# Kernel optimization log

Hardware: AMD Instinct MI355X
Metric: run time of the kernel (lower is better)

Reference implementation:

```python
import jax, jax.numpy as jnp
import numpy as np

B, T, F, U4 = 4096, 72, 64, 1024  # U4 = 4*units, units=256


def setup_inputs() -> dict:
    key = jax.random.key(0)
    ks = jax.random.split(key, 5)
    return {
        "inputs": jax.random.normal(ks[0], (B, T, F), jnp.float32),
        "W": jax.random.normal(ks[1], (F, U4), jnp.float32) * 0.05,   # input kernel [F, 4U]
        "U": jax.random.normal(ks[2], (U4 // 4, U4), jnp.float32) * 0.05,  # recurrent kernel [U, 4U]
        "b": jnp.zeros((U4,), jnp.float32),
        "Wd": jax.random.normal(ks[3], (U4 // 4, F), jnp.float32) * 0.05,  # dense [U, F]
        "bd": jnp.zeros((F,), jnp.float32),
        "out_steps": 24,
    }


def _lstm_step(h, c, x, W, U, b):
    # Keras LSTMCell gate order: i, f, g(candidate), o
    z = x @ W + h @ U + b  # [B, 4U]
    i, f, g, o = jnp.split(z, 4, axis=-1)
    i = jax.nn.sigmoid(i)
    f = jax.nn.sigmoid(f)
    o = jax.nn.sigmoid(o)
    c_new = f * c + i * jnp.tanh(g)
    h_new = o * jnp.tanh(c_new)
    return h_new, c_new


def reference(inputs, W, U, b, Wd, bd, out_steps):
    units = U.shape[0]
    Bt = inputs.shape[0]
    h0 = jnp.zeros((Bt, units), inputs.dtype)
    c0 = jnp.zeros((Bt, units), inputs.dtype)

    # ---- warmup: run RNN over the input sequence ----
    def warm_body(carry, x_t):
        h, c = carry
        h, c = _lstm_step(h, c, x_t, W, U, b)
        return (h, c), None

    (h, c), _ = jax.lax.scan(warm_body, (h0, c0), jnp.swapaxes(inputs, 0, 1))
    pred0 = h @ Wd + bd  # [B, F]

    def dec_body(carry, _):
        pred, h, c = carry
        h, c = _lstm_step(h, c, pred, W, U, b)
        pred = h @ Wd + bd
        return (pred, h, c), pred

    _, preds_rest = jax.lax.scan(dec_body, (pred0, h, c), None, length=out_steps - 1)
    preds = jnp.concatenate([pred0[None], preds_rest], axis=0)  # [out_steps, B, F]
    return jnp.transpose(preds, (1, 0, 2))  # [B, out_steps, F]
```

## Files before the change

kernel.cpp:

```cpp
#include <hip/hip_runtime.h>
#include <math.h>

constexpr int SEQ_T = 72;
constexpr int FDIM  = 64;
constexpr int UNITS = 256;
constexpr int U4    = 1024;
constexpr int BATCH = 4096;
constexpr int NKC   = 10;


constexpr int A_SH    = NKC * 4 * 64 * 8;
constexpr int WL_SH   = 6 * 4 * 4 * 64 * 8;
constexpr int HST_SH  = 2 * 4 * 64 * 8;
constexpr int LDS_BYTES = (A_SH + WL_SH + HST_SH) * 2;

using bf16x8 = __attribute__((ext_vector_type(8))) short;
using f32x4  = __attribute__((ext_vector_type(4))) float;

__device__ __forceinline__ float sigmoid_fast(float x) {
    return 1.0f / (1.0f + __expf(-x));
}
__device__ __forceinline__ float tanh_fast(float x) {
    float ax = fabsf(x);
    float e  = __expf(2.0f * ax);
    float t  = 1.0f - 2.0f / (e + 1.0f);
    return copysignf(t, x);
}
__device__ __forceinline__ unsigned short f2bf(float f) {
    union { float f; unsigned u; } v; v.f = f;
    unsigned r = (v.u + 0x7FFFu + ((v.u >> 16) & 1u)) >> 16;
    return (unsigned short)r;
}
__device__ __forceinline__ bf16x8 pack8(float4 a, float4 b) {
    bf16x8 p;
    p[0] = (short)f2bf(a.x); p[1] = (short)f2bf(a.y);
    p[2] = (short)f2bf(a.z); p[3] = (short)f2bf(a.w);
    p[4] = (short)f2bf(b.x); p[5] = (short)f2bf(b.y);
    p[6] = (short)f2bf(b.z); p[7] = (short)f2bf(b.w);
    return p;
}

__global__ void prep_wblob(const float* __restrict__ W, const float* __restrict__ U,
                           unsigned short* __restrict__ Wblob) {
    int id = blockIdx.x * 256 + threadIdx.x;
    int l    = id & 63;
    int g    = (id >> 6) & 3;
    int ug   = (id >> 8) & 3;
    int rest = id >> 10;
    int kc   = rest % 10, ub = rest / 10;
    int col  = g * 256 + ub * 64 + ug * 16 + (l & 15);
    int kb   = kc * 32 + (l >> 4) * 8;
    bf16x8 v;
    #pragma unroll
    for (int e = 0; e < 8; ++e) {
        int k = kb + e;
        float f = (k < FDIM) ? W[(size_t)k * U4 + col] : U[(size_t)(k - FDIM) * U4 + col];
        v[e] = (short)f2bf(f);
    }
    *reinterpret_cast<bf16x8*>(Wblob + (size_t)id * 8) = v;
}

__global__ void prep_wdblob(const float* __restrict__ Wd, unsigned short* __restrict__ Wdblob) {
    int id = blockIdx.x * 256 + threadIdx.x;
    int l   = id & 63;
    int kcd = (id >> 6) & 7;
    int ft  = id >> 9;
    int f   = ft * 16 + (l & 15);
    int kb  = kcd * 32 + (l >> 4) * 8;
    bf16x8 v;
    #pragma unroll
    for (int e = 0; e < 8; ++e)
        v[e] = (short)f2bf(Wd[(size_t)(kb + e) * FDIM + f]);
    *reinterpret_cast<bf16x8*>(Wdblob + (size_t)id * 8) = v;
}

__device__ __forceinline__ unsigned long long agload(const unsigned long long* p) {
    return __hip_atomic_load(p, __ATOMIC_RELAXED, __HIP_MEMORY_SCOPE_AGENT);
}
__device__ __forceinline__ void agstore(unsigned long long* p, unsigned long long v) {
    __hip_atomic_store(p, v, __ATOMIC_RELAXED, __HIP_MEMORY_SCOPE_AGENT);
}

__global__ __launch_bounds__(512, 1) void lstm_persistent(
    const float* __restrict__ inputs,
    const float* __restrict__ bias,
    const unsigned short* __restrict__ Wblob,
    const unsigned short* __restrict__ Wdblob,
    const float* __restrict__ bd,
    unsigned short* __restrict__ hbuf,
    unsigned int* __restrict__ barcnt,
    float* __restrict__ out,
    int out_steps)
{
    extern __shared__ char smem[];
    unsigned short* A_s = (unsigned short*)smem;
    unsigned short* WL  = (unsigned short*)(smem + A_SH * 2);
    unsigned short* hst = (unsigned short*)(smem + (A_SH + WL_SH) * 2);

    const int tid  = threadIdx.x;
    const int w    = tid >> 6, lane = tid & 63;
    const int l16  = lane & 15, hi4 = lane >> 4;
    const int blk  = blockIdx.x;
    const int rg   = blk & 63, ub = blk >> 6;
    const int bb   = rg * 64;
    const int ug   = w & 3;
    const int m4a  = 2 * (w >> 2);

    {
        const unsigned short* src = Wblob + (size_t)(ub * 10) * 16 * 512;
        #pragma unroll
        for (int i = 0; i < 12; ++i) {
            int idx = (i * 512 + tid) * 8;
            *reinterpret_cast<bf16x8*>(WL + idx) =
                *reinterpret_cast<const bf16x8*>(src + idx);
        }
    }
    bf16x8 Breg[4][4];
    #pragma unroll
    for (int i = 0; i < 4; ++i)
        #pragma unroll
        for (int g = 0; g < 4; ++g)
            Breg[i][g] = *reinterpret_cast<const bf16x8*>(
                Wblob + ((size_t)(((ub * 10 + 6 + i) * 4 + ug) * 4 + g) * 64 + lane) * 8);

    const int uu = ub * 64 + ug * 16 + l16;
    float bz[4];
    #pragma unroll
    for (int g = 0; g < 4; ++g) bz[g] = bias[g * 256 + uu];
    const float bdv = bd[(w & 3) * 16 + l16];

    float c_reg[2][4];
    #pragma unroll
    for (int m = 0; m < 2; ++m)
        #pragma unroll
        for (int j = 0; j < 4; ++j) c_reg[m][j] = 0.0f;

    const int tmax = SEQ_T + out_steps - 1;
    const size_t HB = (size_t)64 * 16384;

    #pragma unroll 1
    for (int t = 0; ; ++t) {
        const int p = t & 1;

        if (t == 0) {
            #pragma unroll
            for (int i = 0; i < 8; ++i)
                *reinterpret_cast<unsigned long long*>(A_s + 4096 + (i * 512 + tid) * 4) = 0ull;
        } else {
            const unsigned long long* src = reinterpret_cast<const unsigned long long*>(
                hbuf + p * HB + (size_t)rg * 16384);
            unsigned long long vbuf[8];
            #pragma unroll
            for (int i = 0; i < 8; ++i) vbuf[i] = agload(src + (size_t)i * 512 + tid);
            #pragma unroll
            for (int i = 0; i < 8; ++i)
                *reinterpret_cast<unsigned long long*>(A_s + 4096 + (i * 512 + tid) * 4) = vbuf[i];
        }
        if (t < SEQ_T) {
            int r = tid >> 3, c8 = (tid & 7) * 8;
            const float* xr = inputs + ((size_t)(bb + r) * SEQ_T + t) * FDIM + c8;
            bf16x8 pk = pack8(*reinterpret_cast<const float4*>(xr),
                              *reinterpret_cast<const float4*>(xr + 4));
            int kcx = c8 >> 5;
            int lb  = (r & 15) | ((((c8 & 31) >> 3) & 3) << 4);
            *reinterpret_cast<bf16x8*>(A_s + ((kcx * 4 + (r >> 4)) * 64 + lb) * 8) = pk;
            __syncthreads();
        } else {
            __syncthreads();
            const int s = t - SEQ_T;
            const int f = (w & 3) * 16 + l16;
            f32x4 accp[2] = {{0.f,0.f,0.f,0.f},{0.f,0.f,0.f,0.f}};
            #pragma unroll
            for (int kcd = 0; kcd < 8; ++kcd) {
                bf16x8 bw = *reinterpret_cast<const bf16x8*>(
                    Wdblob + (size_t)((((w & 3) * 8 + kcd) * 64) + lane) * 8);
                #pragma unroll
                for (int m = 0; m < 2; ++m) {
                    bf16x8 a = *reinterpret_cast<const bf16x8*>(
                        A_s + (((2 + kcd) * 4 + (m4a + m)) * 64 + lane) * 8);
                    accp[m] = __builtin_amdgcn_mfma_f32_16x16x32_bf16(a, bw, accp[m], 0, 0, 0);
                }
            }
            const int kcx = f >> 5;
            const int lsh = (((f & 31) >> 3) & 3) << 4;
            #pragma unroll
            for (int m = 0; m < 2; ++m) {
                #pragma unroll
                for (int j = 0; j < 4; ++j) {
                    int row = (m4a + m) * 16 + hi4 * 4 + j;
                    float v = accp[m][j] + bdv;
                    if (ub == 0)
                        out[((size_t)(bb + row) * out_steps + s) * FDIM + f] = v;
                    A_s[((kcx * 4 + (row >> 4)) * 64 + ((row & 15) | lsh)) * 8 + (f & 7)] = f2bf(v);
                }
            }
            if (t == tmax) break;
            __syncthreads();
        }

        f32x4 acc[2][4];
        #pragma unroll
        for (int m = 0; m < 2; ++m)
            #pragma unroll
            for (int g = 0; g < 4; ++g) acc[m][g] = (f32x4){0.f, 0.f, 0.f, 0.f};

        #pragma unroll
        for (int kc = 0; kc < NKC; ++kc) {
            bf16x8 a0 = *reinterpret_cast<const bf16x8*>(
                A_s + ((kc * 4 + m4a) * 64 + lane) * 8);
            bf16x8 a1 = *reinterpret_cast<const bf16x8*>(
                A_s + ((kc * 4 + m4a + 1) * 64 + lane) * 8);
            #pragma unroll
            for (int g = 0; g < 4; ++g) {
                bf16x8 bw = (kc < 6)
                    ? *reinterpret_cast<const bf16x8*>(
                          WL + (((kc * 4 + ug) * 4 + g) * 64 + lane) * 8)
                    : Breg[kc - 6][g];
                acc[0][g] = __builtin_amdgcn_mfma_f32_16x16x32_bf16(a0, bw, acc[0][g], 0, 0, 0);
                acc[1][g] = __builtin_amdgcn_mfma_f32_16x16x32_bf16(a1, bw, acc[1][g], 0, 0, 0);
            }
        }

        const int kcb = (w & 3) >> 1;
        const int lsh2 = ((((w & 3) & 1) * 2 + (l16 >> 3)) & 3) << 4;
        #pragma unroll
        for (int m = 0; m < 2; ++m) {
            #pragma unroll
            for (int j = 0; j < 4; ++j) {
                float zi = acc[m][0][j] + bz[0];
                float zf = acc[m][1][j] + bz[1];
                float zg = acc[m][2][j] + bz[2];
                float zo = acc[m][3][j] + bz[3];
                float ig = sigmoid_fast(zi);
                float fg = sigmoid_fast(zf);
                float og = sigmoid_fast(zo);
                float cn = fg * c_reg[m][j] + ig * tanh_fast(zg);
                c_reg[m][j] = cn;
                float hv = og * tanh_fast(cn);
                int rl = hi4 * 4 + j;
                hst[((kcb * 4 + (m4a + m)) * 64 + (rl | lsh2)) * 8 + (l16 & 7)] = f2bf(hv);
            }
        }
        __syncthreads();

        {
            unsigned long long* dst = reinterpret_cast<unsigned long long*>(
                hbuf + (1 - p) * HB + (size_t)rg * 16384 + (size_t)(2 * ub) * 2048);
            const unsigned long long* src = reinterpret_cast<const unsigned long long*>(hst);
            agstore(dst + tid,       src[tid]);
            agstore(dst + 512 + tid, src[512 + tid]);
        }

        __syncthreads();
        if (tid == 0) {
            unsigned int* cnt = barcnt + rg * 32;
            __hip_atomic_fetch_add(cnt, 1u, __ATOMIC_RELAXED, __HIP_MEMORY_SCOPE_AGENT);
            const unsigned target = 4u * (unsigned)(t + 1);
            while (__hip_atomic_load(cnt, __ATOMIC_RELAXED, __HIP_MEMORY_SCOPE_AGENT) < target)
                __builtin_amdgcn_s_sleep(2);
        }
        __syncthreads();
    }
}

extern "C" void kernel_launch(void* const* d_in, const int* in_sizes, int n_in,
                              void* d_out, int out_size, void* d_ws, size_t ws_size,
                              hipStream_t stream) {
    const float* inputs = (const float*)d_in[0];
    const float* W      = (const float*)d_in[1];
    const float* U      = (const float*)d_in[2];
    const float* b      = (const float*)d_in[3];
    const float* Wd     = (const float*)d_in[4];
    const float* bd     = (const float*)d_in[5];
    float* out = (float*)d_out;

    const int out_steps = out_size / (BATCH * FDIM);

    char* ws = (char*)d_ws;
    unsigned short* Wblob  = (unsigned short*)(ws);
    unsigned short* Wdblob = (unsigned short*)(ws + (1u << 20));
    unsigned short* hbuf   = (unsigned short*)(ws + (2u << 20));
    unsigned int*   barcnt = (unsigned int*)(ws + (6u << 20));

    prep_wblob<<<160, 256, 0, stream>>>(W, U, Wblob);
    prep_wdblob<<<8, 256, 0, stream>>>(Wd, Wdblob);
    hipMemsetAsync(barcnt, 0, 64 * 128, stream);

    (void)hipFuncSetAttribute((const void*)lstm_persistent,
                              hipFuncAttributeMaxDynamicSharedMemorySize, LDS_BYTES);

    lstm_persistent<<<dim3(256), dim3(512), LDS_BYTES, stream>>>(
        inputs, b, Wblob, Wdblob, bd, hbuf, barcnt, out, out_steps);
}
```

Before: 562.0 us.

## Double threads per block, fold log2e into weights, keep own h slice locally

Each block now runs 1024 threads (16 waves) in place of 512, so every wave handles one 16-row M tile rather than two. This halves per-wave MFMA and activation work and cuts register pressure. Weights and bias are pre-scaled by log2(e) so the gate activations use exp2 plus a hardware reciprocal instead of expf and a division. Each block also writes its own h slice straight into LDS and skips reloading it from global memory, and input staging is reworked for the wider block. The trade-off is a larger block, an extra __syncthreads, and approximate rcp that could shift numerics slightly.

```diff
diff --git a/kernel.cpp b/kernel.cpp
--- a/kernel.cpp
+++ b/kernel.cpp
@@ -7,6 +7,7 @@
 constexpr int U4    = 1024;
 constexpr int BATCH = 4096;
 constexpr int NKC   = 10;
+constexpr float LOG2E = 1.4426950408889634f;
 
 
 constexpr int A_SH    = NKC * 4 * 64 * 8;
@@ -15,29 +16,25 @@
 constexpr int LDS_BYTES = (A_SH + WL_SH + HST_SH) * 2;
 
 using bf16x8 = __attribute__((ext_vector_type(8))) short;
+using bf16x4 = __attribute__((ext_vector_type(4))) short;
 using f32x4  = __attribute__((ext_vector_type(4))) float;
-
-__device__ __forceinline__ float sigmoid_fast(float x) {
-    return 1.0f / (1.0f + __expf(-x));
-}
-__device__ __forceinline__ float tanh_fast(float x) {
-    float ax = fabsf(x);
-    float e  = __expf(2.0f * ax);
-    float t  = 1.0f - 2.0f / (e + 1.0f);
+using ull    = unsigned long long;
+
+__device__ __forceinline__ float sig2(float x) {
+    return __builtin_amdgcn_rcpf(1.0f + exp2f(-x));
+}
+__device__ __forceinline__ float tanh2(float x) {
+    float t = 1.0f - 2.0f * __builtin_amdgcn_rcpf(exp2f(2.0f * fabsf(x)) + 1.0f);
+    return copysignf(t, x);
+}
+__device__ __forceinline__ float tanhc(float x) {
+    float t = 1.0f - 2.0f * __builtin_amdgcn_rcpf(exp2f(2.0f * LOG2E * fabsf(x)) + 1.0f);
     return copysignf(t, x);
 }
 __device__ __forceinline__ unsigned short f2bf(float f) {
     union { float f; unsigned u; } v; v.f = f;
     unsigned r = (v.u + 0x7FFFu + ((v.u >> 16) & 1u)) >> 16;
     return (unsigned short)r;
-}
-__device__ __forceinline__ bf16x8 pack8(float4 a, float4 b) {
-    bf16x8 p;
-    p[0] = (short)f2bf(a.x); p[1] = (short)f2bf(a.y);
-    p[2] = (short)f2bf(a.z); p[3] = (short)f2bf(a.w);
-    p[4] = (short)f2bf(b.x); p[5] = (short)f2bf(b.y);
-    p[6] = (short)f2bf(b.z); p[7] = (short)f2bf(b.w);
-    return p;
 }
 
 __global__ void prep_wblob(const float* __restrict__ W, const float* __restrict__ U,
@@ -55,7 +52,7 @@
     for (int e = 0; e < 8; ++e) {
         int k = kb + e;
         float f = (k < FDIM) ? W[(size_t)k * U4 + col] : U[(size_t)(k - FDIM) * U4 + col];
-        v[e] = (short)f2bf(f);
+        v[e] = (short)f2bf(f * LOG2E);
     }
     *reinterpret_cast<bf16x8*>(Wblob + (size_t)id * 8) = v;
 }
@@ -74,14 +71,14 @@
     *reinterpret_cast<bf16x8*>(Wdblob + (size_t)id * 8) = v;
 }
 
-__device__ __forceinline__ unsigned long long agload(const unsigned long long* p) {
+__device__ __forceinline__ ull agload(const ull* p) {
     return __hip_atomic_load(p, __ATOMIC_RELAXED, __HIP_MEMORY_SCOPE_AGENT);
 }
-__device__ __forceinline__ void agstore(unsigned long long* p, unsigned long long v) {
+__device__ __forceinline__ void agstore(ull* p, ull v) {
     __hip_atomic_store(p, v, __ATOMIC_RELAXED, __HIP_MEMORY_SCOPE_AGENT);
 }
 
-__global__ __launch_bounds__(512, 1) void lstm_persistent(
+__global__ __launch_bounds__(1024) void lstm_persistent(
     const float* __restrict__ inputs,
     const float* __restrict__ bias,
     const unsigned short* __restrict__ Wblob,
@@ -104,13 +101,13 @@
     const int rg   = blk & 63, ub = blk >> 6;
     const int bb   = rg * 64;
     const int ug   = w & 3;
-    const int m4a  = 2 * (w >> 2);
+    const int m4   = w >> 2;
 
     {
         const unsigned short* src = Wblob + (size_t)(ub * 10) * 16 * 512;
         #pragma unroll
-        for (int i = 0; i < 12; ++i) {
-            int idx = (i * 512 + tid) * 8;
+        for (int i = 0; i < 6; ++i) {
+            int idx = (i * 1024 + tid) * 8;
             *reinterpret_cast<bf16x8*>(WL + idx) =
                 *reinterpret_cast<const bf16x8*>(src + idx);
         }
@@ -126,14 +123,14 @@
     const int uu = ub * 64 + ug * 16 + l16;
     float bz[4];
     #pragma unroll
-    for (int g = 0; g < 4; ++g) bz[g] = bias[g * 256 + uu];
+    for (int g = 0; g < 4; ++g) bz[g] = bias[g * 256 + uu] * LOG2E;
     const float bdv = bd[(w & 3) * 16 + l16];
 
-    float c_reg[2][4];
-    #pragma unroll
-    for (int m = 0; m < 2; ++m)
-        #pragma unroll
-        for (int j = 0; j < 4; ++j) c_reg[m][j] = 0.0f;
+    float c_reg[4] = {0.f, 0.f, 0.f, 0.f};
+
+    const int kcq  = ug >> 1;
+    const int lb   = (ug & 1) * 2 + (l16 >> 3);
+    const int elem = l16 & 7;
 
     const int tmax = SEQ_T + out_steps - 1;
     const size_t HB = (size_t)64 * 16384;
@@ -144,114 +141,108 @@
 
         if (t == 0) {
             #pragma unroll
-            for (int i = 0; i < 8; ++i)
-                *reinterpret_cast<unsigned long long*>(A_s + 4096 + (i * 512 + tid) * 4) = 0ull;
+            for (int i = 0; i < 4; ++i)
+                *reinterpret_cast<ull*>(A_s + 4096 + (i * 1024 + tid) * 4) = 0ull;
         } else {
-            const unsigned long long* src = reinterpret_cast<const unsigned long long*>(
-                hbuf + p * HB + (size_t)rg * 16384);
-            unsigned long long vbuf[8];
-            #pragma unroll
-            for (int i = 0; i < 8; ++i) vbuf[i] = agload(src + (size_t)i * 512 + tid);
-            #pragma unroll
-            for (int i = 0; i < 8; ++i)
-                *reinterpret_cast<unsigned long long*>(A_s + 4096 + (i * 512 + tid) * 4) = vbuf[i];
-        }
+            const ull* src = reinterpret_cast<const ull*>(hbuf + p * HB + (size_t)rg * 16384);
+            ull vbuf[4];
+            bool use[4];
+            #pragma unroll
+            for (int ii = 0; ii < 4; ++ii) {
+                int lin = ii * 1024 + tid;
+                use[ii] = ((lin >> 10) != ub);
+                if (use[ii]) vbuf[ii] = agload(src + lin);
+            }
+            #pragma unroll
+            for (int ii = 0; ii < 4; ++ii)
+                if (use[ii])
+                    *reinterpret_cast<ull*>(A_s + 4096 + (ii * 1024 + tid) * 4) = vbuf[ii];
+        }
+
         if (t < SEQ_T) {
-            int r = tid >> 3, c8 = (tid & 7) * 8;
-            const float* xr = inputs + ((size_t)(bb + r) * SEQ_T + t) * FDIM + c8;
-            bf16x8 pk = pack8(*reinterpret_cast<const float4*>(xr),
-                              *reinterpret_cast<const float4*>(xr + 4));
-            int kcx = c8 >> 5;
-            int lb  = (r & 15) | ((((c8 & 31) >> 3) & 3) << 4);
-            *reinterpret_cast<bf16x8*>(A_s + ((kcx * 4 + (r >> 4)) * 64 + lb) * 8) = pk;
+            int r = tid >> 4, c4 = (tid & 15) * 4;
+            float4 v = *reinterpret_cast<const float4*>(
+                inputs + ((size_t)(bb + r) * SEQ_T + t) * FDIM + c4);
+            bf16x4 pk;
+            pk[0] = (short)f2bf(v.x); pk[1] = (short)f2bf(v.y);
+            pk[2] = (short)f2bf(v.z); pk[3] = (short)f2bf(v.w);
+            int kcx = c4 >> 5;
+            int lnb = (r & 15) | ((((c4 & 31) >> 3)) << 4);
+            *reinterpret_cast<bf16x4*>(
+                A_s + ((kcx * 4 + (r >> 4)) * 64 + lnb) * 8 + (c4 & 7)) = pk;
             __syncthreads();
         } else {
             __syncthreads();
             const int s = t - SEQ_T;
             const int f = (w & 3) * 16 + l16;
-            f32x4 accp[2] = {{0.f,0.f,0.f,0.f},{0.f,0.f,0.f,0.f}};
+            f32x4 accp = {0.f, 0.f, 0.f, 0.f};
             #pragma unroll
             for (int kcd = 0; kcd < 8; ++kcd) {
+                bf16x8 a = *reinterpret_cast<const bf16x8*>(
+                    A_s + (((2 + kcd) * 4 + m4) * 64 + lane) * 8);
                 bf16x8 bw = *reinterpret_cast<const bf16x8*>(
                     Wdblob + (size_t)((((w & 3) * 8 + kcd) * 64) + lane) * 8);
-                #pragma unroll
-                for (int m = 0; m < 2; ++m) {
-                    bf16x8 a = *reinterpret_cast<const bf16x8*>(
-                        A_s + (((2 + kcd) * 4 + (m4a + m)) * 64 + lane) * 8);
-                    accp[m] = __builtin_amdgcn_mfma_f32_16x16x32_bf16(a, bw, accp[m], 0, 0, 0);
-                }
+                accp = __builtin_amdgcn_mfma_f32_16x16x32_bf16(a, bw, accp, 0, 0, 0);
             }
             const int kcx = f >> 5;
-            const int lsh = (((f & 31) >> 3) & 3) << 4;
-            #pragma unroll
-            for (int m = 0; m < 2; ++m) {
-                #pragma unroll
-                for (int j = 0; j < 4; ++j) {
-                    int row = (m4a + m) * 16 + hi4 * 4 + j;
-                    float v = accp[m][j] + bdv;
-                    if (ub == 0)
-                        out[((size_t)(bb + row) * out_steps + s) * FDIM + f] = v;
-                    A_s[((kcx * 4 + (row >> 4)) * 64 + ((row & 15) | lsh)) * 8 + (f & 7)] = f2bf(v);
-                }
+            const int lshf = (((f & 31) >> 3)) << 4;
+            #pragma unroll
+            for (int j = 0; j < 4; ++j) {
+                int row = m4 * 16 + hi4 * 4 + j;
+                float v = accp[j] + bdv;
+                if (ub == 0)
+                    out[((size_t)(bb + row) * out_steps + s) * FDIM + f] = v;
+                A_s[((kcx * 4 + m4) * 64 + ((row & 15) | lshf)) * 8 + (f & 7)] = f2bf(v);
             }
             if (t == tmax) break;
             __syncthreads();
         }
 
-        f32x4 acc[2][4];
-        #pragma unroll
-        for (int m = 0; m < 2; ++m)
-            #pragma unroll
-            for (int g = 0; g < 4; ++g) acc[m][g] = (f32x4){0.f, 0.f, 0.f, 0.f};
+        f32x4 acc[4];
+        #pragma unroll
+        for (int g = 0; g < 4; ++g) acc[g] = (f32x4){0.f, 0.f, 0.f, 0.f};
 
         #pragma unroll
         for (int kc = 0; kc < NKC; ++kc) {
-            bf16x8 a0 = *reinterpret_cast<const bf16x8*>(
-                A_s + ((kc * 4 + m4a) * 64 + lane) * 8);
-            bf16x8 a1 = *reinterpret_cast<const bf16x8*>(
-                A_s + ((kc * 4 + m4a + 1) * 64 + lane) * 8);
+            bf16x8 a = *reinterpret_cast<const bf16x8*>(
+                A_s + ((kc * 4 + m4) * 64 + lane) * 8);
             #pragma unroll
             for (int g = 0; g < 4; ++g) {
                 bf16x8 bw = (kc < 6)
                     ? *reinterpret_cast<const bf16x8*>(
                           WL + (((kc * 4 + ug) * 4 + g) * 64 + lane) * 8)
                     : Breg[kc - 6][g];
-                acc[0][g] = __builtin_amdgcn_mfma_f32_16x16x32_bf16(a0, bw, acc[0][g], 0, 0, 0);
-                acc[1][g] = __builtin_amdgcn_mfma_f32_16x16x32_bf16(a1, bw, acc[1][g], 0, 0, 0);
-            }
-        }
-
-        const int kcb = (w & 3) >> 1;
-        const int lsh2 = ((((w & 3) & 1) * 2 + (l16 >> 3)) & 3) << 4;
-        #pragma unroll
-        for (int m = 0; m < 2; ++m) {
-            #pragma unroll
-            for (int j = 0; j < 4; ++j) {
-                float zi = acc[m][0][j] + bz[0];
-                float zf = acc[m][1][j] + bz[1];
-                float zg = acc[m][2][j] + bz[2];
-                float zo = acc[m][3][j] + bz[3];
-                float ig = sigmoid_fast(zi);
-                float fg = sigmoid_fast(zf);
-                float og = sigmoid_fast(zo);
-                float cn = fg * c_reg[m][j] + ig * tanh_fast(zg);
-                c_reg[m][j] = cn;
-                float hv = og * tanh_fast(cn);
-                int rl = hi4 * 4 + j;
-                hst[((kcb * 4 + (m4a + m)) * 64 + (rl | lsh2)) * 8 + (l16 & 7)] = f2bf(hv);
-            }
+                acc[g] = __builtin_amdgcn_mfma_f32_16x16x32_bf16(a, bw, acc[g], 0, 0, 0);
+            }
+        }
+        __syncthreads();
+
+        #pragma unroll
+        for (int j = 0; j < 4; ++j) {
+            float zi = acc[0][j] + bz[0];
+            float zf = acc[1][j] + bz[1];
+            float zg = acc[2][j] + bz[2];
+            float zo = acc[3][j] + bz[3];
+            float ig = sig2(zi);
+            float fg = sig2(zf);
+            float og = sig2(zo);
+            float cn = fg * c_reg[j] + ig * tanh2(zg);
+            c_reg[j] = cn;
+            unsigned short hv = f2bf(og * tanhc(cn));
+            int rl = hi4 * 4 + j;
+            int lnb = rl | (lb << 4);
+            hst[((kcq * 4 + m4) * 64 + lnb) * 8 + elem] = hv;
+            A_s[(((2 + 2 * ub + kcq) * 4 + m4) * 64 + lnb) * 8 + elem] = hv;
         }
         __syncthreads();
 
         {
-            unsigned long long* dst = reinterpret_cast<unsigned long long*>(
-                hbuf + (1 - p) * HB + (size_t)rg * 16384 + (size_t)(2 * ub) * 2048);
-            const unsigned long long* src = reinterpret_cast<const unsigned long long*>(hst);
-            agstore(dst + tid,       src[tid]);
-            agstore(dst + 512 + tid, src[512 + tid]);
-        }
-
-        __syncthreads();
+            ull* dst = reinterpret_cast<ull*>(
+                hbuf + (1 - p) * HB + (size_t)rg * 16384 + (size_t)ub * 4096);
+            agstore(dst + tid, reinterpret_cast<const ull*>(hst)[tid]);
+        }
+        __syncthreads();
+
         if (tid == 0) {
             unsigned int* cnt = barcnt + rg * 32;
             __hip_atomic_fetch_add(cnt, 1u, __ATOMIC_RELAXED, __HIP_MEMORY_SCOPE_AGENT);
@@ -289,6 +280,6 @@
     (void)hipFuncSetAttribute((const void*)lstm_persistent,
                               hipFuncAttributeMaxDynamicSharedMemorySize, LDS_BYTES);
 
-    lstm_persistent<<<dim3(256), dim3(512), LDS_BYTES, stream>>>(
+    lstm_persistent<<<dim3(256), dim3(1024), LDS_BYTES, stream>>>(
         inputs, b, Wblob, Wdblob, bd, hbuf, barcnt, out, out_steps);
 }
```

Result: slower. 810.8 us (+44.3%).
